# Performance work log

Measured on AMD Instinct MI355X. Metric: run time of the kernel, lower is better.

The kernel has to match this reference:

```python
import jax, jax.numpy as jnp
import numpy as np

B, T, C = 8, 2048, 1024
NEG_BIG = -1e30  # exp(NEG_BIG - row_max) underflows to exactly 0 in fp32


def setup_inputs() -> dict:
    key = jax.random.key(0)
    k1, k2 = jax.random.split(key)
    x = jax.random.normal(k1, (B, T, C), dtype=jnp.float32)
    # nn.Linear weight, shape [out, in]; forward computes x @ W^T
    W_H = jax.random.normal(k2, (C, C), dtype=jnp.float32) * (1.0 / np.sqrt(C))
    return {"x": x, "W_H": W_H}


def reference(x, W_H):
    Tdim = x.shape[1]
    xH = jnp.einsum('btc,dc->btd', x, W_H)          # H(x) = x @ W^T, [B,T,C]
    scores = jnp.einsum('btc,bsc->bts', x, xH)       # bilinear scores, [B,T,T]
    # tril_plus_one=True -> strictly-lower-triangular mask (diagonal=-1)
    mask = jnp.tril(jnp.ones((Tdim, Tdim), dtype=bool), k=-1)
    scores = jnp.where(mask, scores, NEG_BIG)
    wei = jax.nn.softmax(scores, axis=-1)            # fully-masked rows -> uniform, zeroed below
    all_masked = ~mask.any(axis=-1)                  # [T], True for row 0
    wei = jnp.where(all_masked[None, :, None], 0.0, wei)
    out = jnp.einsum('bts,bsc->btc', wei, xH)
    return -out
```

## Files before the change

### kernel.cpp

```cpp
#include <hip/hip_runtime.h>
#include <stdint.h>

#define Bn 8
#define Tn 2048
#define Cn 1024
#define Mn (Bn * Tn)
#define NTRI 136

typedef __attribute__((ext_vector_type(4))) float f32x4;
typedef _Float16 f16;
typedef __attribute__((ext_vector_type(8))) _Float16 f16x8;
typedef uint16_t u16;
typedef uint32_t u32;

static __device__ __forceinline__ u16 f2h(float f) {
  union { f16 h; u16 u; } c; c.h = (f16)f; return c.u;
}
static __device__ __forceinline__ f32x4 mfmaH(f16x8 a, f16x8 b, f32x4 c) {
  return __builtin_amdgcn_mfma_f32_16x16x32_f16(a, b, c, 0, 0, 0);
}
static __device__ __forceinline__ void gld16(const void* g, void* l) {
  __builtin_amdgcn_global_load_lds(
      (const __attribute__((address_space(1))) u32*)g,
      (__attribute__((address_space(3))) u32*)l, 16, 0, 0);
}


__global__ __launch_bounds__(256) void ksplitW(const float* __restrict__ s,
                                               u16* __restrict__ hi) {
  size_t i = ((size_t)blockIdx.x * 256 + threadIdx.x) * 8;
  float4 a = *(const float4*)(s + i), b = *(const float4*)(s + i + 4);
  float f[8] = {a.x, a.y, a.z, a.w, b.x, b.y, b.z, b.w};
  union { u16 u[8]; uint4 v; } H;
#pragma unroll
  for (int j = 0; j < 8; ++j) H.u[j] = f2h(f[j]);
  *(uint4*)(hi + i) = H.v;
}

__global__ __launch_bounds__(256) void ksplitX(const float* __restrict__ s,
                                               u16* __restrict__ hi,
                                               u16* __restrict__ lo) {
  size_t i = ((size_t)blockIdx.x * 256 + threadIdx.x) * 8;
  float4 a = *(const float4*)(s + i), b = *(const float4*)(s + i + 4);
  float f[8] = {a.x, a.y, a.z, a.w, b.x, b.y, b.z, b.w};
  union { u16 u[8]; uint4 v; } H, L;
#pragma unroll
  for (int j = 0; j < 8; ++j) {
    f16 h = (f16)f[j];
    union { f16 h; u16 u; } ch; ch.h = h;
    H.u[j] = ch.u;
    L.u[j] = f2h(f[j] - (float)h);
  }
  *(uint4*)(hi + i) = H.v;
  *(uint4*)(lo + i) = L.v;
}

__global__ __launch_bounds__(256) void k1_xh(const u16* __restrict__ x_h,
                                             const u16* __restrict__ W_h,
                                             u16* __restrict__ xh) {
  __shared__ __align__(16) u16 Ah[8192], Bh[8192];
  const int tid = threadIdx.x;
  const int m0 = blockIdx.x * 128, n0 = blockIdx.y * 128;
  const int wave = tid >> 6, lane = tid & 63;
  const int wrow = (wave >> 1) * 64, wcol = (wave & 1) * 64;
  const int quad = lane >> 4, l16 = lane & 15;
  const int ssw = ((((tid >> 3) & 3) ^ (tid & 3))) * 8;
  const int qs8 = (quad ^ ((l16 >> 1) & 3)) * 8;

  f32x4 acc[4][4] = {};

  for (int k0 = 0; k0 < Cn; k0 += 64) {
#pragma unroll
    for (int i = 0; i < 4; ++i) {
      int chunk = i * 256 + tid;
      int kk = chunk >> 9, row = (chunk >> 2) & 127;
      gld16(x_h + (size_t)(m0 + row) * Cn + k0 + kk * 32 + ssw, Ah + chunk * 8);
      gld16(W_h + (size_t)(n0 + row) * Cn + k0 + kk * 32 + ssw, Bh + chunk * 8);
    }
    __syncthreads();
#pragma unroll
    for (int kk = 0; kk < 2; ++kk) {
      f16x8 a[4], b[4];
#pragma unroll
      for (int i = 0; i < 4; ++i) {
        a[i] = *(const f16x8*)(Ah + kk * 4096 + (wrow + i * 16 + l16) * 32 + qs8);
        b[i] = *(const f16x8*)(Bh + kk * 4096 + (wcol + i * 16 + l16) * 32 + qs8);
      }
#pragma unroll
      for (int mi = 0; mi < 4; ++mi)
#pragma unroll
        for (int ni = 0; ni < 4; ++ni)
          acc[mi][ni] = mfmaH(a[mi], b[ni], acc[mi][ni]);
    }
    __syncthreads();
  }
#pragma unroll
  for (int mi = 0; mi < 4; ++mi)
#pragma unroll
    for (int ni = 0; ni < 4; ++ni)
#pragma unroll
      for (int r = 0; r < 4; ++r) {
        int row = wrow + mi * 16 + quad * 4 + r;
        int col = wcol + ni * 16 + l16;
        xh[(size_t)(m0 + row) * Cn + n0 + col] = f2h(acc[mi][ni][r]);
      }
}

__global__ __launch_bounds__(512) void k2_scores(const u16* __restrict__ x_h,
                                                 const u16* __restrict__ x_l,
                                                 const u16* __restrict__ xh,
                                                 u16* __restrict__ P,
                                                 float* __restrict__ mt,
                                                 float* __restrict__ lt) {
  __shared__ __align__(16) union {
    struct { u16 Ah[3][4096], Al[3][4096], Bh[3][8192]; } s;
    struct { float Mrow[4][128]; float Lrow[4][128]; } e;
  } u;
  const int tid = threadIdx.x;

  const int bid = blockIdx.x;
  const int half = gridDim.x / 144;
  const int xcd = bid & 7, slot = bid >> 3;
  const int p = xcd & 3, h = xcd >> 2;
  const int n1 = 16 - 2 * p, n2 = 2 * p + 2;
  int c, j, bb;
  if (slot < n1 * half) {
    c = p; bb = slot / n1; j = slot % n1;
  } else {
    int s2 = slot - n1 * half; c = 7 - p; bb = s2 / n2; j = s2 % n2;
  }
  const int bL = h * half + bb;
  const int qt = 2 * c + j, bcol = c;
  const int t0 = qt * 128, s0 = bcol * 256;

  const int wave = tid >> 6, lane = tid & 63;
  const int wc = wave & 3;
  const int wrow = (wave >> 2) * 64, wcol = wc * 64;
  const int quad = lane >> 4, l16 = lane & 15;
  const int ssw = ((((tid >> 3) & 3) ^ (tid & 3))) * 8;
  const int qs8 = (quad ^ ((l16 >> 1) & 3)) * 8;

  f32x4 acc[4][4] = {};
  const size_t abase = ((size_t)bL * Tn + t0) * Cn;
  const size_t bbase = ((size_t)bL * Tn + s0) * Cn;
  const int arow = tid >> 2;

  auto stage = [&](int buf, int k0) {
    size_t aoff = abase + (size_t)arow * Cn + k0 + ssw;
    gld16(x_h + aoff, &u.s.Ah[buf][tid * 8]);
    gld16(x_l + aoff, &u.s.Al[buf][tid * 8]);
#pragma unroll
    for (int i = 0; i < 2; ++i) {
      int ch = i * 512 + tid;
      int row = ch >> 2;
      gld16(xh + bbase + (size_t)row * Cn + k0 + ssw, &u.s.Bh[buf][ch * 8]);
    }
  };

  stage(0, 0);
  stage(1, 32);
  int cur = 0;
#pragma unroll 1
  for (int kidx = 0; kidx < 32; ++kidx) {
    if (kidx < 31) {
      asm volatile("s_waitcnt vmcnt(4) lgkmcnt(0)" ::: "memory");
    } else {
      asm volatile("s_waitcnt vmcnt(0) lgkmcnt(0)" ::: "memory");
    }
    __builtin_amdgcn_s_barrier();
    __builtin_amdgcn_sched_barrier(0);
    if (kidx < 30) {
      int tgt = cur >= 1 ? cur - 1 : 2;
      stage(tgt, (kidx + 2) * 32);
    }
    f16x8 b[4];
#pragma unroll
    for (int ni = 0; ni < 4; ++ni)
      b[ni] = *(const f16x8*)&u.s.Bh[cur][(wcol + ni * 16 + l16) * 32 + qs8];
#pragma unroll
    for (int mi = 0; mi < 4; ++mi) {
      f16x8 ah = *(const f16x8*)&u.s.Ah[cur][(wrow + mi * 16 + l16) * 32 + qs8];
      f16x8 al = *(const f16x8*)&u.s.Al[cur][(wrow + mi * 16 + l16) * 32 + qs8];
#pragma unroll
      for (int ni = 0; ni < 4; ++ni) {
        acc[mi][ni] = mfmaH(ah, b[ni], acc[mi][ni]);
        acc[mi][ni] = mfmaH(al, b[ni], acc[mi][ni]);
      }
    }
    cur = cur < 2 ? cur + 1 : 0;
  }

  float rm[4][4];
#pragma unroll
  for (int mi = 0; mi < 4; ++mi)
#pragma unroll
    for (int r = 0; r < 4; ++r) {
      int row = wrow + mi * 16 + quad * 4 + r;
      float m = -1e30f;
#pragma unroll
      for (int ni = 0; ni < 4; ++ni) {
        int scol = s0 + wcol + ni * 16 + l16;
        if (scol >= t0 + row) acc[mi][ni][r] = -1e30f;
        m = fmaxf(m, acc[mi][ni][r]);
      }
      m = fmaxf(m, __shfl_xor(m, 1));
      m = fmaxf(m, __shfl_xor(m, 2));
      m = fmaxf(m, __shfl_xor(m, 4));
      m = fmaxf(m, __shfl_xor(m, 8));
      rm[mi][r] = m;
    }
  if (l16 == 0) {
#pragma unroll
    for (int mi = 0; mi < 4; ++mi)
#pragma unroll
      for (int r = 0; r < 4; ++r)
        u.e.Mrow[wc][wrow + mi * 16 + quad * 4 + r] = rm[mi][r];
  }
  __syncthreads();
  const int h2 = (wc >> 1) * 2;
  float rs[4][4];
#pragma unroll
  for (int mi = 0; mi < 4; ++mi)
#pragma unroll
    for (int r = 0; r < 4; ++r) {
      int row = wrow + mi * 16 + quad * 4 + r;
      float m2 = fmaxf(u.e.Mrow[h2][row], u.e.Mrow[h2 + 1][row]);
      float s = 0.f;
#pragma unroll
      for (int ni = 0; ni < 4; ++ni) {
        int scol = s0 + wcol + ni * 16 + l16;
        float pv = (scol < t0 + row) ? __expf(acc[mi][ni][r] - m2) : 0.0f;
        acc[mi][ni][r] = pv;
        s += pv;
      }
      s += __shfl_xor(s, 1);
      s += __shfl_xor(s, 2);
      s += __shfl_xor(s, 4);
      s += __shfl_xor(s, 8);
      rs[mi][r] = s;
      rm[mi][r] = m2;
    }
  if (l16 == 0) {
#pragma unroll
    for (int mi = 0; mi < 4; ++mi)
#pragma unroll
      for (int r = 0; r < 4; ++r)
        u.e.Lrow[wc][wrow + mi * 16 + quad * 4 + r] = rs[mi][r];
  }
  __syncthreads();
  const int st128 = bcol * 2 + (wc >> 1);
  if (st128 <= qt) {
    if ((wc & 1) == 0 && l16 == 0) {
#pragma unroll
      for (int mi = 0; mi < 4; ++mi)
#pragma unroll
        for (int r = 0; r < 4; ++r) {
          int row = wrow + mi * 16 + quad * 4 + r;
          size_t rI = (size_t)bL * Tn + t0 + row;
          mt[rI * 16 + st128] = rm[mi][r];
          lt[rI * 16 + st128] = u.e.Lrow[wc][row] + u.e.Lrow[wc + 1][row];
        }
    }
    const size_t pbase = (size_t)(bL * NTRI + qt * (qt + 1) / 2 + st128) * 16384;
#pragma unroll
    for (int mi = 0; mi < 4; ++mi)
#pragma unroll
      for (int ni = 0; ni < 4; ++ni)
#pragma unroll
        for (int r = 0; r < 4; ++r) {
          int row = wrow + mi * 16 + quad * 4 + r;
          int pcol = (wcol & 64) + ni * 16 + l16;
          P[pbase + row * 128 + pcol] = f2h(acc[mi][ni][r]);
        }
  }
}

__global__ __launch_bounds__(256) void k3_stats(const float* __restrict__ mt,
                                                const float* __restrict__ lt,
                                                float* __restrict__ Mr,
                                                float* __restrict__ Li) {
  int r = blockIdx.x * 256 + threadIdx.x;
  int t = r & (Tn - 1);
  int nt = (t == 0) ? 0 : (((t - 1) >> 7) + 1);
  float M = -1e30f;
  for (int i = 0; i < nt; ++i) M = fmaxf(M, mt[(size_t)r * 16 + i]);
  float L = 0.f;
  for (int i = 0; i < nt; ++i) L += lt[(size_t)r * 16 + i] * __expf(mt[(size_t)r * 16 + i] - M);
  Mr[r] = M;
  Li[r] = (L > 0.f) ? 1.f / L : 0.f;
}

__global__ __launch_bounds__(256) void ktr(const u16* __restrict__ src,
                                           u16* __restrict__ dst) {
  __shared__ __align__(16) u16 S[128 * 136];
  const int t0 = blockIdx.x * 128, c0 = blockIdx.y * 128, b = blockIdx.z;
  const int tid = threadIdx.x;
#pragma unroll
  for (int i = 0; i < 8; ++i) {
    int chunk = tid + i * 256;
    int row = chunk >> 4, c8 = (chunk & 15) * 8;
    uint4 v = *(const uint4*)(src + ((size_t)b * Tn + t0 + row) * Cn + c0 + c8);
    *(uint4*)(S + row * 136 + c8) = v;
  }
  __syncthreads();
#pragma unroll
  for (int i = 0; i < 8; ++i) {
    int chunk = tid + i * 256;
    int crow = chunk >> 4, t8 = (chunk & 15) * 8;
    union { u16 s[8]; uint4 v; } o;
#pragma unroll
    for (int j = 0; j < 8; ++j) o.s[j] = S[(t8 + j) * 136 + crow];
    *(uint4*)(dst + ((size_t)b * Cn + c0 + crow) * Tn + t0 + t8) = o.v;
  }
}

__global__ __launch_bounds__(512) void k4_out(const u16* __restrict__ P,
                                              const u16* __restrict__ xhT,
                                              const float* __restrict__ mt,
                                              const float* __restrict__ Mr,
                                              const float* __restrict__ Li,
                                              float* __restrict__ out) {
  __shared__ __align__(16) u16 Ap[3][4096], Bp[3][8192];
  __shared__ u16 alphaLds[16 * 128];
  const int tid = threadIdx.x;
  const int tt = 15 - blockIdx.x;
  const int cn = blockIdx.y, bL = blockIdx.z;
  const int t0 = tt * 128, c0 = cn * 256;
  const int wave = tid >> 6, lane = tid & 63;
  const int wc = wave & 3;
  const int wrow = (wave >> 2) * 64, wcol = wc * 64;
  const int quad = lane >> 4, l16 = lane & 15;
  const int ssw = ((((tid >> 3) & 3) ^ (tid & 3))) * 8;
  const int qs8 = (quad ^ ((l16 >> 1) & 3)) * 8;

  {
    const size_t rbase = (size_t)bL * Tn + t0;
#pragma unroll
    for (int j = 0; j < 4; ++j) {
      int idx = tid + j * 512;
      int stp = idx >> 7, row = idx & 127;
      float a = 0.f;
      if (stp <= tt)
        a = __expf(mt[(rbase + row) * 16 + stp] - Mr[rbase + row]) * Li[rbase + row];
      alphaLds[idx] = f2h(a);
    }
  }

  f32x4 acc[4][4] = {};
  const size_t bbase = ((size_t)bL * Cn + c0) * Tn;
  const size_t ptile0 = (size_t)(bL * NTRI + tt * (tt + 1) / 2) * 16384;

  auto stage = [&](int buf, int step) {
    const int st = step >> 2, k32 = (step & 3) * 32;
    {
      int row = tid >> 2;
      gld16(P + ptile0 + (size_t)st * 16384 + row * 128 + k32 + ssw,
            &Ap[buf][tid * 8]);
    }
#pragma unroll
    for (int i = 0; i < 2; ++i) {
      int ch = i * 512 + tid;
      int row = ch >> 2;
      gld16(xhT + bbase + (size_t)row * Tn + st * 128 + k32 + ssw,
            &Bp[buf][ch * 8]);
    }
  };

  const int steps = 4 * (tt + 1);
  stage(0, 0);
  stage(1, 1);
  int cur = 0;
#pragma unroll 1
  for (int s = 0; s < steps; ++s) {
    if (s < steps - 1) {
      asm volatile("s_waitcnt vmcnt(3) lgkmcnt(0)" ::: "memory");
    } else {
      asm volatile("s_waitcnt vmcnt(0) lgkmcnt(0)" ::: "memory");
    }
    __builtin_amdgcn_s_barrier();
    __builtin_amdgcn_sched_barrier(0);
    if (s < steps - 2) {
      int tgt = cur >= 1 ? cur - 1 : 2;
      stage(tgt, s + 2);
    }
    const int st = s >> 2;
    f16x8 b[4];
#pragma unroll
    for (int ni = 0; ni < 4; ++ni)
      b[ni] = *(const f16x8*)&Bp[cur][(wcol + ni * 16 + l16) * 32 + qs8];
#pragma unroll
    for (int mi = 0; mi < 4; ++mi) {
      union { u16 u; f16 h; } ca;
      ca.u = alphaLds[st * 128 + wrow + mi * 16 + l16];
      f16x8 sv;
#pragma unroll
      for (int j = 0; j < 8; ++j) sv[j] = ca.h;
      f16x8 a = *(const f16x8*)&Ap[cur][(wrow + mi * 16 + l16) * 32 + qs8];
      a = a * sv;
#pragma unroll
      for (int ni = 0; ni < 4; ++ni)
        acc[mi][ni] = mfmaH(a, b[ni], acc[mi][ni]);
    }
    cur = cur < 2 ? cur + 1 : 0;
  }

#pragma unroll
  for (int mi = 0; mi < 4; ++mi)
#pragma unroll
    for (int ni = 0; ni < 4; ++ni)
#pragma unroll
      for (int r = 0; r < 4; ++r) {
        int row = wrow + mi * 16 + quad * 4 + r;
        int col = wcol + ni * 16 + l16;
        out[((size_t)bL * Tn + t0 + row) * Cn + c0 + col] = -acc[mi][ni][r];
      }
}

extern "C" void kernel_launch(void* const* d_in, const int* in_sizes, int n_in,
                              void* d_out, int out_size, void* d_ws, size_t ws_size,
                              hipStream_t stream) {
  (void)in_sizes; (void)n_in; (void)out_size;
  const float* x = (const float*)d_in[0];
  const float* W = (const float*)d_in[1];
  float* out = (float*)d_out;

  const size_t FULL_NEED = 3ull * Mn * Cn * 2 + (size_t)Bn * NTRI * 16384 * 2 +
                           (size_t)Cn * Cn * 2 + 2ull * Mn * 16 * 4 + 2ull * Mn * 4;
  const int nch = (ws_size >= FULL_NEED) ? 1 : 2;
  const int nb = Bn / nch;
  const size_t rowsC = (size_t)nb * Tn;
  const size_t sA = rowsC * Cn * 2;

  char* p = (char*)d_ws;
  u16* x_h = (u16*)p; p += sA;
  u16* xLT = (u16*)p; p += sA;
  u16* xh  = (u16*)p; p += sA;
  u16* Pp  = (u16*)p; p += (size_t)nb * NTRI * 16384 * 2;
  u16* W_h = (u16*)p; p += (size_t)Cn * Cn * 2;
  float* mt = (float*)p; p += rowsC * 16 * 4;
  float* lt = (float*)p; p += rowsC * 16 * 4;
  float* Mr = (float*)p; p += rowsC * 4;
  float* Li = (float*)p; p += rowsC * 4;

  dim3 blk(256);
  ksplitW<<<dim3(Cn * Cn / 2048), blk, 0, stream>>>(W, W_h);
  for (int c = 0; c < nch; ++c) {
    const float* xc = x + (size_t)c * rowsC * Cn;
    float* oc = out + (size_t)c * rowsC * Cn;
    ksplitX<<<dim3((u32)(rowsC * Cn / 2048)), blk, 0, stream>>>(xc, x_h, xLT);
    k1_xh<<<dim3((u32)(rowsC / 128), Cn / 128), blk, 0, stream>>>(x_h, W_h, xh);
    k2_scores<<<dim3(72 * nb), dim3(512), 0, stream>>>(x_h, xLT, xh, Pp, mt, lt);
    k3_stats<<<dim3((u32)(rowsC / 256)), blk, 0, stream>>>(mt, lt, Mr, Li);
    ktr<<<dim3(Tn / 128, Cn / 128, nb), blk, 0, stream>>>(xh, xLT);
    k4_out<<<dim3(16, Cn / 256, nb), dim3(512), 0, stream>>>(Pp, xLT, mt, Mr, Li, oc);
  }
}
```

Measured before the change: 365.9 us.

## Enlarge scores tile to 256x256 per block and drop cross-wave softmax reduction

The scores kernel now computes a 256x256 tile per block instead of 128x256, with each wave owning a 64x128 subtile (8 MFMA columns). Each wave computes its own row max and sum for its 128-column P tile, so the shared-memory exchange and two block barriers for partial stats are gone. The block count halves and the triangular schedule changes to 36 tiles per batch. This raises operand reuse per staged byte but increases accumulator registers and LDS use (three 8K buffers per operand), which may reduce occupancy, and diagonal tiles now compute more masked-out work.

After: 394.0 us. 7.7% more time.

```diff
diff --git a/kernel.cpp b/kernel.cpp
--- a/kernel.cpp
+++ b/kernel.cpp
@@ -112,48 +112,40 @@
                                                  u16* __restrict__ P,
                                                  float* __restrict__ mt,
                                                  float* __restrict__ lt) {
-  __shared__ __align__(16) union {
-    struct { u16 Ah[3][4096], Al[3][4096], Bh[3][8192]; } s;
-    struct { float Mrow[4][128]; float Lrow[4][128]; } e;
-  } u;
+  __shared__ __align__(16) u16 Ah[3][8192], Al[3][8192], Bh[3][8192];
   const int tid = threadIdx.x;
 
   const int bid = blockIdx.x;
-  const int half = gridDim.x / 144;
+  const int half = gridDim.x / 72;
   const int xcd = bid & 7, slot = bid >> 3;
   const int p = xcd & 3, h = xcd >> 2;
-  const int n1 = 16 - 2 * p, n2 = 2 * p + 2;
-  int c, j, bb;
-  if (slot < n1 * half) {
-    c = p; bb = slot / n1; j = slot % n1;
-  } else {
-    int s2 = slot - n1 * half; c = 7 - p; bb = s2 / n2; j = s2 % n2;
-  }
+  const int bb = slot / 9, j = slot % 9;
   const int bL = h * half + bb;
-  const int qt = 2 * c + j, bcol = c;
-  const int t0 = qt * 128, s0 = bcol * 256;
+  const int n1 = 8 - p;
+  const int bcol2 = (j < n1) ? p : 7 - p;
+  const int qt2   = (j < n1) ? p + j : (7 - p) + (j - n1);
+  const int t0 = qt2 * 256, s0 = bcol2 * 256;
 
   const int wave = tid >> 6, lane = tid & 63;
-  const int wc = wave & 3;
-  const int wrow = (wave >> 2) * 64, wcol = wc * 64;
+  const int wr = wave >> 1, wcl = wave & 1;
+  const int wrow = wr * 64, wcol = wcl * 128;
   const int quad = lane >> 4, l16 = lane & 15;
   const int ssw = ((((tid >> 3) & 3) ^ (tid & 3))) * 8;
   const int qs8 = (quad ^ ((l16 >> 1) & 3)) * 8;
 
-  f32x4 acc[4][4] = {};
+  f32x4 acc[4][8] = {};
   const size_t abase = ((size_t)bL * Tn + t0) * Cn;
   const size_t bbase = ((size_t)bL * Tn + s0) * Cn;
-  const int arow = tid >> 2;
+  const int srow = tid >> 2;
 
   auto stage = [&](int buf, int k0) {
-    size_t aoff = abase + (size_t)arow * Cn + k0 + ssw;
-    gld16(x_h + aoff, &u.s.Ah[buf][tid * 8]);
-    gld16(x_l + aoff, &u.s.Al[buf][tid * 8]);
 #pragma unroll
     for (int i = 0; i < 2; ++i) {
-      int ch = i * 512 + tid;
-      int row = ch >> 2;
-      gld16(xh + bbase + (size_t)row * Cn + k0 + ssw, &u.s.Bh[buf][ch * 8]);
+      size_t off = (size_t)(i * 128 + srow) * Cn + k0 + ssw;
+      int dst = (i * 512 + tid) * 8;
+      gld16(x_h + abase + off, &Ah[buf][dst]);
+      gld16(x_l + abase + off, &Al[buf][dst]);
+      gld16(xh  + bbase + off, &Bh[buf][dst]);
     }
   };
 
@@ -163,7 +155,7 @@
 #pragma unroll 1
   for (int kidx = 0; kidx < 32; ++kidx) {
     if (kidx < 31) {
-      asm volatile("s_waitcnt vmcnt(4) lgkmcnt(0)" ::: "memory");
+      asm volatile("s_waitcnt vmcnt(6) lgkmcnt(0)" ::: "memory");
     } else {
       asm volatile("s_waitcnt vmcnt(0) lgkmcnt(0)" ::: "memory");
     }
@@ -173,16 +165,16 @@
       int tgt = cur >= 1 ? cur - 1 : 2;
       stage(tgt, (kidx + 2) * 32);
     }
-    f16x8 b[4];
-#pragma unroll
-    for (int ni = 0; ni < 4; ++ni)
-      b[ni] = *(const f16x8*)&u.s.Bh[cur][(wcol + ni * 16 + l16) * 32 + qs8];
+    f16x8 b[8];
+#pragma unroll
+    for (int ni = 0; ni < 8; ++ni)
+      b[ni] = *(const f16x8*)&Bh[cur][(wcol + ni * 16 + l16) * 32 + qs8];
 #pragma unroll
     for (int mi = 0; mi < 4; ++mi) {
-      f16x8 ah = *(const f16x8*)&u.s.Ah[cur][(wrow + mi * 16 + l16) * 32 + qs8];
-      f16x8 al = *(const f16x8*)&u.s.Al[cur][(wrow + mi * 16 + l16) * 32 + qs8];
-#pragma unroll
-      for (int ni = 0; ni < 4; ++ni) {
+      f16x8 ah = *(const f16x8*)&Ah[cur][(wrow + mi * 16 + l16) * 32 + qs8];
+      f16x8 al = *(const f16x8*)&Al[cur][(wrow + mi * 16 + l16) * 32 + qs8];
+#pragma unroll
+      for (int ni = 0; ni < 8; ++ni) {
         acc[mi][ni] = mfmaH(ah, b[ni], acc[mi][ni]);
         acc[mi][ni] = mfmaH(al, b[ni], acc[mi][ni]);
       }
@@ -190,7 +182,11 @@
     cur = cur < 2 ? cur + 1 : 0;
   }
 
-  float rm[4][4];
+  const int qt128 = 2 * qt2 + (wr >> 1);
+  const int st128 = 2 * bcol2 + wcl;
+  const bool valid = st128 <= qt128;
+  const size_t pbase = (size_t)(bL * NTRI + qt128 * (qt128 + 1) / 2 + st128) * 16384;
+
 #pragma unroll
   for (int mi = 0; mi < 4; ++mi)
 #pragma unroll
@@ -198,7 +194,7 @@
       int row = wrow + mi * 16 + quad * 4 + r;
       float m = -1e30f;
 #pragma unroll
-      for (int ni = 0; ni < 4; ++ni) {
+      for (int ni = 0; ni < 8; ++ni) {
         int scol = s0 + wcol + ni * 16 + l16;
         if (scol >= t0 + row) acc[mi][ni][r] = -1e30f;
         m = fmaxf(m, acc[mi][ni][r]);
@@ -207,29 +203,11 @@
       m = fmaxf(m, __shfl_xor(m, 2));
       m = fmaxf(m, __shfl_xor(m, 4));
       m = fmaxf(m, __shfl_xor(m, 8));
-      rm[mi][r] = m;
-    }
-  if (l16 == 0) {
-#pragma unroll
-    for (int mi = 0; mi < 4; ++mi)
-#pragma unroll
-      for (int r = 0; r < 4; ++r)
-        u.e.Mrow[wc][wrow + mi * 16 + quad * 4 + r] = rm[mi][r];
-  }
-  __syncthreads();
-  const int h2 = (wc >> 1) * 2;
-  float rs[4][4];
-#pragma unroll
-  for (int mi = 0; mi < 4; ++mi)
-#pragma unroll
-    for (int r = 0; r < 4; ++r) {
-      int row = wrow + mi * 16 + quad * 4 + r;
-      float m2 = fmaxf(u.e.Mrow[h2][row], u.e.Mrow[h2 + 1][row]);
       float s = 0.f;
 #pragma unroll
-      for (int ni = 0; ni < 4; ++ni) {
+      for (int ni = 0; ni < 8; ++ni) {
         int scol = s0 + wcol + ni * 16 + l16;
-        float pv = (scol < t0 + row) ? __expf(acc[mi][ni][r] - m2) : 0.0f;
+        float pv = (scol < t0 + row) ? __expf(acc[mi][ni][r] - m) : 0.0f;
         acc[mi][ni][r] = pv;
         s += pv;
       }
@@ -237,40 +215,22 @@
       s += __shfl_xor(s, 2);
       s += __shfl_xor(s, 4);
       s += __shfl_xor(s, 8);
-      rs[mi][r] = s;
-      rm[mi][r] = m2;
-    }
-  if (l16 == 0) {
+      if (valid && l16 == 0) {
+        size_t rI = (size_t)bL * Tn + t0 + row;
+        mt[rI * 16 + st128] = m;
+        lt[rI * 16 + st128] = s;
+      }
+    }
+  if (valid) {
 #pragma unroll
     for (int mi = 0; mi < 4; ++mi)
 #pragma unroll
-      for (int r = 0; r < 4; ++r)
-        u.e.Lrow[wc][wrow + mi * 16 + quad * 4 + r] = rs[mi][r];
-  }
-  __syncthreads();
-  const int st128 = bcol * 2 + (wc >> 1);
-  if (st128 <= qt) {
-    if ((wc & 1) == 0 && l16 == 0) {
-#pragma unroll
-      for (int mi = 0; mi < 4; ++mi)
+      for (int ni = 0; ni < 8; ++ni)
 #pragma unroll
         for (int r = 0; r < 4; ++r) {
-          int row = wrow + mi * 16 + quad * 4 + r;
-          size_t rI = (size_t)bL * Tn + t0 + row;
-          mt[rI * 16 + st128] = rm[mi][r];
-          lt[rI * 16 + st128] = u.e.Lrow[wc][row] + u.e.Lrow[wc + 1][row];
-        }
-    }
-    const size_t pbase = (size_t)(bL * NTRI + qt * (qt + 1) / 2 + st128) * 16384;
-#pragma unroll
-    for (int mi = 0; mi < 4; ++mi)
-#pragma unroll
-      for (int ni = 0; ni < 4; ++ni)
-#pragma unroll
-        for (int r = 0; r < 4; ++r) {
-          int row = wrow + mi * 16 + quad * 4 + r;
-          int pcol = (wcol & 64) + ni * 16 + l16;
-          P[pbase + row * 128 + pcol] = f2h(acc[mi][ni][r]);
+          int row128 = (wrow & 64) + mi * 16 + quad * 4 + r;
+          int pcol = ni * 16 + l16;
+          P[pbase + row128 * 128 + pcol] = f2h(acc[mi][ni][r]);
         }
   }
 }
@@ -449,7 +409,7 @@
     float* oc = out + (size_t)c * rowsC * Cn;
     ksplitX<<<dim3((u32)(rowsC * Cn / 2048)), blk, 0, stream>>>(xc, x_h, xLT);
     k1_xh<<<dim3((u32)(rowsC / 128), Cn / 128), blk, 0, stream>>>(x_h, W_h, xh);
-    k2_scores<<<dim3(72 * nb), dim3(512), 0, stream>>>(x_h, xLT, xh, Pp, mt, lt);
+    k2_scores<<<dim3(36 * nb), dim3(512), 0, stream>>>(x_h, xLT, xh, Pp, mt, lt);
     k3_stats<<<dim3((u32)(rowsC / 256)), blk, 0, stream>>>(mt, lt, Mr, Li);
     ktr<<<dim3(Tn / 128, Cn / 128, nb), blk, 0, stream>>>(xh, xLT);
     k4_out<<<dim3(16, Cn / 256, nb), dim3(512), 0, stream>>>(Pp, xLT, mt, Mr, Li, oc);
```
